# Kernel tuning notes

Hardware: AMD Instinct MI355X
Metric: run time of the kernel (lower is better)

The kernel has to match this reference:

```python
import jax, jax.numpy as jnp
import numpy as np

B, S, D, H, HD = 4096, 50, 32, 4, 8
SCALE = 1.0 / (8 ** 0.5)


def setup_inputs() -> dict:
    key = jax.random.key(0)
    ks = jax.random.split(key, 12)
    inp = {
        'Q': jax.random.normal(ks[0], (B, S, D), dtype=jnp.float32),
        'K': jax.random.normal(ks[1], (B, S, D), dtype=jnp.float32),
        'V': jax.random.normal(ks[2], (B, S, D), dtype=jnp.float32),
        'mask': jax.random.randint(ks[3], (B, 1, S, S), 0, 2).astype(jnp.bool_),
        # Linear weights (stored as [in, out]; equivalent math to torch's x @ W.T + b)
        'WQ': jax.random.normal(ks[4], (D, D), dtype=jnp.float32) * 0.1,
        'bQ': jnp.zeros((D,), dtype=jnp.float32),
        'WK': jax.random.normal(ks[5], (D, D), dtype=jnp.float32) * 0.1,
        'bK': jnp.zeros((D,), dtype=jnp.float32),
        'WV': jax.random.normal(ks[6], (D, D), dtype=jnp.float32) * 0.1,
        'bV': jnp.zeros((D,), dtype=jnp.float32),
        'WO': jax.random.normal(ks[7], (D, D), dtype=jnp.float32) * 0.1,
        'bO': jnp.zeros((D,), dtype=jnp.float32),
    }
    return inp


def reference(Q, K, V, mask, WQ, bQ, WK, bK, WV, bV, WO, bO):
    qSrc = Q
    # fcQ/fcK/fcV are (faithfully) applied twice, as in the original forward
    q = (Q @ WQ + bQ) @ WQ + bQ
    k = (K @ WK + bK) @ WK + bK
    v = (V @ WV + bV) @ WV + bV
    # split heads: [B, S, D] -> [B, H, S, HD]
    q = q.reshape(B, S, H, HD).transpose(0, 2, 1, 3)
    k = k.reshape(B, S, H, HD).transpose(0, 2, 1, 3)
    v = v.reshape(B, S, H, HD).transpose(0, 2, 1, 3)
    score = jnp.einsum('bhqd,bhkd->bhqk', q, k) * SCALE
    score = jnp.where(mask, -jnp.inf, score)
    attn = jax.nn.softmax(score, axis=-1)
    ctx = jnp.einsum('bhqk,bhkd->bhqd', attn, v)
    ctx = ctx.transpose(0, 2, 1, 3).reshape(B, S, D)
    out = ctx @ WO + bO  # dropout is identity in eval mode
    return qSrc + out
```

## Files before the change

### kernel.cpp

```cpp
#include <hip/hip_runtime.h>

#define NB 4096
constexpr float kQscale = 0.35355339059327378f * 1.4426950408889634f;

constexpr int ST = 40;
constexpr int SP = 72;
constexpr int SV = 72;
constexpr int OFF_W  = 0;
constexpr int OFF_V2 = 0;
constexpr int OFF_A  = 5120;
constexpr int OFF_C  = 7680;
constexpr int OFF_B  = 10240;
constexpr int SH_LEN = 12800;

typedef __attribute__((ext_vector_type(8))) short bf16x8;
typedef __attribute__((ext_vector_type(4))) float f32x4;

__device__ __forceinline__ unsigned cvt2(float lo, float hi) {
  unsigned u;
  asm("v_cvt_pk_bf16_f32 %0, %1, %2" : "=v"(u) : "v"(lo), "v"(hi));
  return u;
}
__device__ __forceinline__ float fexp2(float x) {
  float r;
  asm("v_exp_f32 %0, %1" : "=v"(r) : "v"(x));
  return r;
}

__global__ __launch_bounds__(256) void mha(
    const float* __restrict__ Qg, const float* __restrict__ Kg,
    const float* __restrict__ Vg, const void* __restrict__ maskg,
    const float* __restrict__ WQg, const float* __restrict__ bQg,
    const float* __restrict__ WKg, const float* __restrict__ bKg,
    const float* __restrict__ WVg, const float* __restrict__ bVg,
    const float* __restrict__ WOg, const float* __restrict__ bOg,
    float* __restrict__ outg)
{
  __shared__ __align__(16) short SH[SH_LEN];
  __shared__ __align__(16) float sBias[128];
  __shared__ unsigned sRaw[80];
  __shared__ unsigned sMask[128];

  const int t = threadIdx.x;
  const int b = blockIdx.x;
  const int lane = t & 63;
  const int wv = t >> 6;
  const int c = lane & 15, g = lane >> 4;
  const int myrow = wv*16 + c;

  auto stage_tile = [&](const float* __restrict__ src, int dstOff) {
    #pragma unroll
    for (int it = 0; it < 2; ++it) {
      const int idx = t + it*256;
      if (idx < 400) {
        const float4 x = ((const float4*)src)[idx];
        const int s = idx >> 3, qd = idx & 7;
        *(uint2*)&SH[dstOff + s*ST + qd*4] = make_uint2(cvt2(x.x, x.y), cvt2(x.z, x.w));
      }
    }
  };

  auto projStep = [&](bf16x8 xb, int wm, int biasOff, int yOff, float scale) {
    #pragma unroll
    for (int Ni = 0; Ni < 2; ++Ni) {
      const bf16x8 wa = *(const bf16x8*)&SH[OFF_W + wm*1280 + (Ni*16 + c)*ST + g*8];
      const float4 bv = *(const float4*)&sBias[biasOff + Ni*16 + g*4];
      f32x4 acc = {bv.x, bv.y, bv.z, bv.w};
      acc = __builtin_amdgcn_mfma_f32_16x16x32_bf16(wa, xb, acc, 0, 0, 0);
      *(uint2*)&SH[yOff + myrow*ST + Ni*16 + g*4] =
          make_uint2(cvt2(acc[0]*scale, acc[1]*scale), cvt2(acc[2]*scale, acc[3]*scale));
    }
  };

  const unsigned w64det = ((const unsigned*)maskg)[lane];
  unsigned valB[10];
  #pragma unroll
  for (int cc = 0; cc < 10; ++cc) {
    const int idx = (wv*10 + cc)*64 + lane;
    valB[cc] = (idx < 2500) ? (unsigned)((const unsigned char*)maskg)[b*2500 + idx] : 0u;
  }
  stage_tile(Kg + b*1600, OFF_A);
  stage_tile(Qg + b*1600, OFF_C);
  stage_tile(Vg + b*1600, OFF_B);
  #pragma unroll
  for (int m = 0; m < 4; ++m) {
    const float* Wp = (m == 0) ? WQg : (m == 1) ? WKg : (m == 2) ? WVg : WOg;
    const float4 x = ((const float4*)Wp)[t];
    const int k = t >> 3, d0 = (t & 7)*4;
    const unsigned u0 = cvt2(x.x, x.y), u1 = cvt2(x.z, x.w);
    SH[OFF_W + m*1280 + (d0+0)*ST + k] = (short)(u0 & 0xFFFF);
    SH[OFF_W + m*1280 + (d0+1)*ST + k] = (short)(u0 >> 16);
    SH[OFF_W + m*1280 + (d0+2)*ST + k] = (short)(u1 & 0xFFFF);
    SH[OFF_W + m*1280 + (d0+3)*ST + k] = (short)(u1 >> 16);
  }
  if      (t < 32)  sBias[t] = bQg[t];
  else if (t < 64)  sBias[t] = bKg[t-32];
  else if (t < 96)  sBias[t] = bVg[t-64];
  else if (t < 128) sBias[t] = bOg[t-96];
  {
    const bool byteMask = (__ballot(w64det > 1u) != 0ull);
    #pragma unroll
    for (int cc = 0; cc < 10; ++cc) {
      const int ch = wv*10 + cc;
      const int idx = ch*64 + lane;
      unsigned val;
      if (byteMask) val = valB[cc];
      else          val = (idx < 2500) ? ((const unsigned*)maskg)[b*2500 + idx] : 0u;
      const unsigned long long m = __ballot(val != 0u);
      if (lane == 0) {
        sRaw[ch*2]     = (unsigned)m;
        sRaw[ch*2 + 1] = (unsigned)(m >> 32);
      }
    }
  }
  __syncthreads();

  if (t < 100) {
    const int i = t >> 1, half = t & 1;
    const int bitpos = 50*i + half*32;
    const int a = bitpos >> 5, sh = bitpos & 31;
    unsigned w = sRaw[a] >> sh;
    if (sh) w |= sRaw[a+1] << (32 - sh);
    sMask[t] = w;
  }
  {
    const bf16x8 aK = *(const bf16x8*)&SH[OFF_A + myrow*ST + g*8];
    const bf16x8 aV = *(const bf16x8*)&SH[OFF_B + myrow*ST + g*8];
    const bf16x8 aQ = *(const bf16x8*)&SH[OFF_C + myrow*ST + g*8];
    projStep(aK, 1, 32, OFF_A, 1.f);
    projStep(aV, 2, 64, OFF_B, 1.f);
    projStep(aQ, 0, 0,  OFF_C, 1.f);
  }
  f32x4 vacc0, vacc1;
  {
    const bf16x8 aK = *(const bf16x8*)&SH[OFF_A + myrow*ST + g*8];
    const bf16x8 aV = *(const bf16x8*)&SH[OFF_B + myrow*ST + g*8];
    const bf16x8 aQ = *(const bf16x8*)&SH[OFF_C + myrow*ST + g*8];
    projStep(aK, 1, 32, OFF_A, 1.f);
    projStep(aQ, 0, 0, OFF_C, kQscale);
    {
      const bf16x8 b0 = *(const bf16x8*)&SH[OFF_W + 2*1280 + c*ST + g*8];
      const bf16x8 b1 = *(const bf16x8*)&SH[OFF_W + 2*1280 + (16 + c)*ST + g*8];
      const float bv0 = sBias[64 + c], bv1 = sBias[64 + 16 + c];
      f32x4 z0 = {bv0, bv0, bv0, bv0}, z1 = {bv1, bv1, bv1, bv1};
      vacc0 = __builtin_amdgcn_mfma_f32_16x16x32_bf16(aV, b0, z0, 0, 0, 0);
      vacc1 = __builtin_amdgcn_mfma_f32_16x16x32_bf16(aV, b1, z1, 0, 0, 0);
    }
  }
  __syncthreads();

  {
    const int j0 = wv*16 + g*4;
    const float v0 = (j0+0 < 50) ? vacc0[0] : 0.f;
    const float v1 = (j0+1 < 50) ? vacc0[1] : 0.f;
    const float v2 = (j0+2 < 50) ? vacc0[2] : 0.f;
    const float v3 = (j0+3 < 50) ? vacc0[3] : 0.f;
    *(uint2*)&SH[OFF_V2 + c*SV + j0] = make_uint2(cvt2(v0,v1), cvt2(v2,v3));
    const float u0 = (j0+0 < 50) ? vacc1[0] : 0.f;
    const float u1 = (j0+1 < 50) ? vacc1[1] : 0.f;
    const float u2 = (j0+2 < 50) ? vacc1[2] : 0.f;
    const float u3 = (j0+3 < 50) ? vacc1[3] : 0.f;
    *(uint2*)&SH[OFF_V2 + (16 + c)*SV + j0] = make_uint2(cvt2(u0,u1), cvt2(u2,u3));
  }
  const bf16x8 qb = *(const bf16x8*)&SH[OFF_C + myrow*ST + g*8];
  bf16x8 kf[4];
  #pragma unroll
  for (int Ni = 0; Ni < 4; ++Ni)
    kf[Ni] = *(const bf16x8*)&SH[OFF_A + (Ni*16 + c)*ST + g*8];
  const unsigned m0 = (myrow < 50) ? sMask[myrow*2]     : 0xFFFFFFFFu;
  const unsigned m1 = (myrow < 50) ? sMask[myrow*2 + 1] : 0xFFFFFFFFu;
  const bf16x8 zf = {0,0,0,0,0,0,0,0};

  auto qkt_exp = [&](int h, unsigned pk[8], float& ri) {
    const bf16x8 qh = (g == h) ? qb : zf;
    float rs = 0.f;
    #pragma unroll
    for (int Ni = 0; Ni < 4; ++Ni) {
      f32x4 z = {0.f, 0.f, 0.f, 0.f};
      const f32x4 s = __builtin_amdgcn_mfma_f32_16x16x32_bf16(kf[Ni], qh, z, 0, 0, 0);
      const unsigned w = (Ni < 2) ? m0 : m1;
      float p[4];
      #pragma unroll
      for (int r = 0; r < 4; ++r) {
        const int key = Ni*16 + g*4 + r;
        const bool keep = (key < 50) && (((w >> (key & 31)) & 1u) == 0u);
        p[r] = keep ? fexp2(s[r]) : 0.f;
        rs += p[r];
      }
      pk[Ni*2]   = cvt2(p[0], p[1]);
      pk[Ni*2+1] = cvt2(p[2], p[3]);
    }
    rs += __shfl_xor(rs, 16);
    rs += __shfl_xor(rs, 32);
    ri = __builtin_amdgcn_rcpf(rs);
  };

  unsigned pkA[8]; float riA;
  qkt_exp(0, pkA, riA);
  __syncthreads();

  short* SPp = &SH[OFF_A];
  #pragma unroll
  for (int h = 0; h < 4; ++h) {
    #pragma unroll
    for (int Ni = 0; Ni < 4; ++Ni)
      *(uint2*)&SPp[myrow*SP + Ni*16 + g*4] = make_uint2(pkA[Ni*2], pkA[Ni*2+1]);
    const bf16x8 vf0 = *(const bf16x8*)&SH[OFF_V2 + (h*8 + (c & 7))*SV + g*8];
    const bf16x8 vf1 = *(const bf16x8*)&SH[OFF_V2 + (h*8 + (c & 7))*SV + 32 + g*8];
    unsigned pkN[8] = {0,0,0,0,0,0,0,0}; float riN = 0.f;
    if (h < 3) qkt_exp(h+1, pkN, riN);
    const bf16x8 pf0 = *(const bf16x8*)&SPp[myrow*SP + g*8];
    const bf16x8 pf1 = *(const bf16x8*)&SPp[myrow*SP + 32 + g*8];
    f32x4 cac = {0.f, 0.f, 0.f, 0.f};
    cac = __builtin_amdgcn_mfma_f32_16x16x32_bf16(vf0, pf0, cac, 0, 0, 0);
    cac = __builtin_amdgcn_mfma_f32_16x16x32_bf16(vf1, pf1, cac, 0, 0, 0);
    if (g < 2)
      *(uint2*)&SH[OFF_B + myrow*ST + h*8 + g*4] =
          make_uint2(cvt2(cac[0]*riA, cac[1]*riA), cvt2(cac[2]*riA, cac[3]*riA));
    #pragma unroll
    for (int e = 0; e < 8; ++e) pkA[e] = pkN[e];
    riA = riN;
  }

  {
    float res[2][4];
    #pragma unroll
    for (int Nj = 0; Nj < 2; ++Nj)
      #pragma unroll
      for (int r = 0; r < 4; ++r) {
        const int row = wv*16 + g*4 + r;
        res[Nj][r] = (row < 50) ? Qg[b*1600 + row*32 + Nj*16 + c] : 0.f;
      }
    const bf16x8 af = *(const bf16x8*)&SH[OFF_B + myrow*ST + g*8];
    #pragma unroll
    for (int Nj = 0; Nj < 2; ++Nj) {
      const bf16x8 bbf = *(const bf16x8*)&SH[OFF_W + 3*1280 + (Nj*16 + c)*ST + g*8];
      const float bv = sBias[96 + Nj*16 + c];
      f32x4 o = {bv, bv, bv, bv};
      o = __builtin_amdgcn_mfma_f32_16x16x32_bf16(af, bbf, o, 0, 0, 0);
      #pragma unroll
      for (int r = 0; r < 4; ++r) {
        const int row = wv*16 + g*4 + r;
        if (row < 50)
          outg[b*1600 + row*32 + Nj*16 + c] = o[r] + res[Nj][r];
      }
    }
  }
}

extern "C" void kernel_launch(void* const* d_in, const int* in_sizes, int n_in,
                              void* d_out, int out_size, void* d_ws, size_t ws_size,
                              hipStream_t stream) {
  const float* Q  = (const float*)d_in[0];
  const float* K  = (const float*)d_in[1];
  const float* V  = (const float*)d_in[2];
  const void*  M  = d_in[3];
  const float* WQ = (const float*)d_in[4];
  const float* bQ = (const float*)d_in[5];
  const float* WK = (const float*)d_in[6];
  const float* bK = (const float*)d_in[7];
  const float* WV = (const float*)d_in[8];
  const float* bV = (const float*)d_in[9];
  const float* WO = (const float*)d_in[10];
  const float* bO = (const float*)d_in[11];
  float* out = (float*)d_out;
  (void)d_ws; (void)ws_size; (void)in_sizes; (void)n_in; (void)out_size;

  hipLaunchKernelGGL(mha, dim3(NB), dim3(256), 0, stream,
                     Q, K, V, M, WQ, bQ, WK, bK, WV, bV, WO, bO, out);
}
```

Measured before the change: 57.74 us.

## Transpose P and context in registers via permlane swaps instead of LDS

Replaces the shared-memory round trip for the softmax probability matrix and the per-head context output with in-register cross-lane exchanges using v_permlane32/16_swap. The bit mask for each row is now extracted per thread straight from the raw ballot words, which removes the separate sMask staging pass, and weight staging uses coalesced column reads with packed 8-byte LDS stores. This cuts LDS traffic, bank conflicts and one pipelined prefetch structure, but drops the software pipelining of QK^T with PV and relies on the permlane lane mapping being correct.

```diff
diff --git a/kernel.cpp b/kernel.cpp
--- a/kernel.cpp
+++ b/kernel.cpp
@@ -4,7 +4,6 @@
 constexpr float kQscale = 0.35355339059327378f * 1.4426950408889634f;
 
 constexpr int ST = 40;
-constexpr int SP = 72;
 constexpr int SV = 72;
 constexpr int OFF_W  = 0;
 constexpr int OFF_V2 = 0;
@@ -15,6 +14,7 @@
 
 typedef __attribute__((ext_vector_type(8))) short bf16x8;
 typedef __attribute__((ext_vector_type(4))) float f32x4;
+typedef __attribute__((ext_vector_type(4))) unsigned u32x4;
 
 __device__ __forceinline__ unsigned cvt2(float lo, float hi) {
   unsigned u;
@@ -25,6 +25,10 @@
   float r;
   asm("v_exp_f32 %0, %1" : "=v"(r) : "v"(x));
   return r;
+}
+__device__ __forceinline__ void xchF(unsigned& a, unsigned& b) {
+  asm volatile("v_permlane32_swap_b32 %0, %1" : "+v"(a), "+v"(b));
+  asm volatile("v_permlane16_swap_b32 %0, %1" : "+v"(a), "+v"(b));
 }
 
 __global__ __launch_bounds__(256) void mha(
@@ -39,7 +43,6 @@
   __shared__ __align__(16) short SH[SH_LEN];
   __shared__ __align__(16) float sBias[128];
   __shared__ unsigned sRaw[80];
-  __shared__ unsigned sMask[128];
 
   const int t = threadIdx.x;
   const int b = blockIdx.x;
@@ -82,16 +85,17 @@
   stage_tile(Kg + b*1600, OFF_A);
   stage_tile(Qg + b*1600, OFF_C);
   stage_tile(Vg + b*1600, OFF_B);
-  #pragma unroll
-  for (int m = 0; m < 4; ++m) {
-    const float* Wp = (m == 0) ? WQg : (m == 1) ? WKg : (m == 2) ? WVg : WOg;
-    const float4 x = ((const float4*)Wp)[t];
-    const int k = t >> 3, d0 = (t & 7)*4;
-    const unsigned u0 = cvt2(x.x, x.y), u1 = cvt2(x.z, x.w);
-    SH[OFF_W + m*1280 + (d0+0)*ST + k] = (short)(u0 & 0xFFFF);
-    SH[OFF_W + m*1280 + (d0+1)*ST + k] = (short)(u0 >> 16);
-    SH[OFF_W + m*1280 + (d0+2)*ST + k] = (short)(u1 & 0xFFFF);
-    SH[OFF_W + m*1280 + (d0+3)*ST + k] = (short)(u1 >> 16);
+  {
+    const int wd = t & 31, wk0 = (t >> 5) * 4;
+    #pragma unroll
+    for (int m = 0; m < 4; ++m) {
+      const float* Wp = (m == 0) ? WQg : (m == 1) ? WKg : (m == 2) ? WVg : WOg;
+      const float w0 = Wp[(wk0+0)*32 + wd];
+      const float w1 = Wp[(wk0+1)*32 + wd];
+      const float w2 = Wp[(wk0+2)*32 + wd];
+      const float w3 = Wp[(wk0+3)*32 + wd];
+      *(uint2*)&SH[OFF_W + m*1280 + wd*ST + wk0] = make_uint2(cvt2(w0,w1), cvt2(w2,w3));
+    }
   }
   if      (t < 32)  sBias[t] = bQg[t];
   else if (t < 64)  sBias[t] = bKg[t-32];
@@ -115,14 +119,6 @@
   }
   __syncthreads();
 
-  if (t < 100) {
-    const int i = t >> 1, half = t & 1;
-    const int bitpos = 50*i + half*32;
-    const int a = bitpos >> 5, sh = bitpos & 31;
-    unsigned w = sRaw[a] >> sh;
-    if (sh) w |= sRaw[a+1] << (32 - sh);
-    sMask[t] = w;
-  }
   {
     const bf16x8 aK = *(const bf16x8*)&SH[OFF_A + myrow*ST + g*8];
     const bf16x8 aV = *(const bf16x8*)&SH[OFF_B + myrow*ST + g*8];
@@ -138,14 +134,12 @@
     const bf16x8 aQ = *(const bf16x8*)&SH[OFF_C + myrow*ST + g*8];
     projStep(aK, 1, 32, OFF_A, 1.f);
     projStep(aQ, 0, 0, OFF_C, kQscale);
-    {
-      const bf16x8 b0 = *(const bf16x8*)&SH[OFF_W + 2*1280 + c*ST + g*8];
-      const bf16x8 b1 = *(const bf16x8*)&SH[OFF_W + 2*1280 + (16 + c)*ST + g*8];
-      const float bv0 = sBias[64 + c], bv1 = sBias[64 + 16 + c];
-      f32x4 z0 = {bv0, bv0, bv0, bv0}, z1 = {bv1, bv1, bv1, bv1};
-      vacc0 = __builtin_amdgcn_mfma_f32_16x16x32_bf16(aV, b0, z0, 0, 0, 0);
-      vacc1 = __builtin_amdgcn_mfma_f32_16x16x32_bf16(aV, b1, z1, 0, 0, 0);
-    }
+    const bf16x8 b0 = *(const bf16x8*)&SH[OFF_W + 2*1280 + c*ST + g*8];
+    const bf16x8 b1 = *(const bf16x8*)&SH[OFF_W + 2*1280 + (16 + c)*ST + g*8];
+    const float bv0 = sBias[64 + c], bv1 = sBias[64 + 16 + c];
+    f32x4 z0 = {bv0, bv0, bv0, bv0}, z1 = {bv1, bv1, bv1, bv1};
+    vacc0 = __builtin_amdgcn_mfma_f32_16x16x32_bf16(aV, b0, z0, 0, 0, 0);
+    vacc1 = __builtin_amdgcn_mfma_f32_16x16x32_bf16(aV, b1, z1, 0, 0, 0);
   }
   __syncthreads();
 
@@ -162,23 +156,38 @@
     const float u3 = (j0+3 < 50) ? vacc1[3] : 0.f;
     *(uint2*)&SH[OFF_V2 + (16 + c)*SV + j0] = make_uint2(cvt2(u0,u1), cvt2(u2,u3));
   }
+  unsigned mm0, mm1;
+  {
+    const int bp = (myrow < 50) ? 50*myrow : 0;
+    const unsigned ra = sRaw[(bp >> 5) + 0];
+    const unsigned rb = sRaw[(bp >> 5) + 1];
+    const unsigned rc = sRaw[(bp >> 5) + 2];
+    const unsigned sh = bp & 31;
+    mm0 = (unsigned)((((unsigned long long)rb << 32) | ra) >> sh);
+    mm1 = (unsigned)((((unsigned long long)rc << 32) | rb) >> sh);
+    if (myrow >= 50) { mm0 = ~0u; mm1 = ~0u; }
+  }
   const bf16x8 qb = *(const bf16x8*)&SH[OFF_C + myrow*ST + g*8];
   bf16x8 kf[4];
   #pragma unroll
   for (int Ni = 0; Ni < 4; ++Ni)
     kf[Ni] = *(const bf16x8*)&SH[OFF_A + (Ni*16 + c)*ST + g*8];
-  const unsigned m0 = (myrow < 50) ? sMask[myrow*2]     : 0xFFFFFFFFu;
-  const unsigned m1 = (myrow < 50) ? sMask[myrow*2 + 1] : 0xFFFFFFFFu;
+  __syncthreads();
+
   const bf16x8 zf = {0,0,0,0,0,0,0,0};
-
-  auto qkt_exp = [&](int h, unsigned pk[8], float& ri) {
+  unsigned ox0[4], ox1[4];
+  #pragma unroll
+  for (int h = 0; h < 4; ++h) {
+    const bf16x8 vf0 = *(const bf16x8*)&SH[OFF_V2 + (h*8 + (c & 7))*SV + g*8];
+    const bf16x8 vf1 = *(const bf16x8*)&SH[OFF_V2 + (h*8 + (c & 7))*SV + 32 + g*8];
     const bf16x8 qh = (g == h) ? qb : zf;
+    unsigned pk[8];
     float rs = 0.f;
     #pragma unroll
     for (int Ni = 0; Ni < 4; ++Ni) {
       f32x4 z = {0.f, 0.f, 0.f, 0.f};
       const f32x4 s = __builtin_amdgcn_mfma_f32_16x16x32_bf16(kf[Ni], qh, z, 0, 0, 0);
-      const unsigned w = (Ni < 2) ? m0 : m1;
+      const unsigned w = (Ni < 2) ? mm0 : mm1;
       float p[4];
       #pragma unroll
       for (int r = 0; r < 4; ++r) {
@@ -192,34 +201,20 @@
     }
     rs += __shfl_xor(rs, 16);
     rs += __shfl_xor(rs, 32);
-    ri = __builtin_amdgcn_rcpf(rs);
-  };
-
-  unsigned pkA[8]; float riA;
-  qkt_exp(0, pkA, riA);
-  __syncthreads();
-
-  short* SPp = &SH[OFF_A];
-  #pragma unroll
-  for (int h = 0; h < 4; ++h) {
-    #pragma unroll
-    for (int Ni = 0; Ni < 4; ++Ni)
-      *(uint2*)&SPp[myrow*SP + Ni*16 + g*4] = make_uint2(pkA[Ni*2], pkA[Ni*2+1]);
-    const bf16x8 vf0 = *(const bf16x8*)&SH[OFF_V2 + (h*8 + (c & 7))*SV + g*8];
-    const bf16x8 vf1 = *(const bf16x8*)&SH[OFF_V2 + (h*8 + (c & 7))*SV + 32 + g*8];
-    unsigned pkN[8] = {0,0,0,0,0,0,0,0}; float riN = 0.f;
-    if (h < 3) qkt_exp(h+1, pkN, riN);
-    const bf16x8 pf0 = *(const bf16x8*)&SPp[myrow*SP + g*8];
-    const bf16x8 pf1 = *(const bf16x8*)&SPp[myrow*SP + 32 + g*8];
+    const float ri = __builtin_amdgcn_rcpf(rs);
+    unsigned w0 = pk[0], w2 = pk[2];  xchF(w0, w2);
+    unsigned w1 = pk[1], w3 = pk[3];  xchF(w1, w3);
+    unsigned x0 = pk[4], x2 = pk[6];  xchF(x0, x2);
+    unsigned x1 = pk[5], x3 = pk[7];  xchF(x1, x3);
+    const u32x4 w0v = {w0, w1, w2, w3};
+    const u32x4 w1v = {x0, x1, x2, x3};
+    const bf16x8 pf0 = __builtin_bit_cast(bf16x8, w0v);
+    const bf16x8 pf1 = __builtin_bit_cast(bf16x8, w1v);
     f32x4 cac = {0.f, 0.f, 0.f, 0.f};
     cac = __builtin_amdgcn_mfma_f32_16x16x32_bf16(vf0, pf0, cac, 0, 0, 0);
     cac = __builtin_amdgcn_mfma_f32_16x16x32_bf16(vf1, pf1, cac, 0, 0, 0);
-    if (g < 2)
-      *(uint2*)&SH[OFF_B + myrow*ST + h*8 + g*4] =
-          make_uint2(cvt2(cac[0]*riA, cac[1]*riA), cvt2(cac[2]*riA, cac[3]*riA));
-    #pragma unroll
-    for (int e = 0; e < 8; ++e) pkA[e] = pkN[e];
-    riA = riN;
+    ox0[h] = cvt2(cac[0]*ri, cac[1]*ri);
+    ox1[h] = cvt2(cac[2]*ri, cac[3]*ri);
   }
 
   {
@@ -231,7 +226,18 @@
         const int row = wv*16 + g*4 + r;
         res[Nj][r] = (row < 50) ? Qg[b*1600 + row*32 + Nj*16 + c] : 0.f;
       }
-    const bf16x8 af = *(const bf16x8*)&SH[OFF_B + myrow*ST + g*8];
+    unsigned a0 = ox0[0], a1 = ox0[1], a2 = ox0[2], a3 = ox0[3];
+    xchF(a0, a1);
+    xchF(a2, a3);
+    xchF(a0, a2);
+    xchF(a1, a3);
+    unsigned c0 = ox1[0], c1 = ox1[1], c2 = ox1[2], c3 = ox1[3];
+    xchF(c0, c1);
+    xchF(c2, c3);
+    xchF(c0, c2);
+    xchF(c1, c3);
+    const u32x4 afv = {a0, c0, a1, c1};
+    const bf16x8 af = __builtin_bit_cast(bf16x8, afv);
     #pragma unroll
     for (int Nj = 0; Nj < 2; ++Nj) {
       const bf16x8 bbf = *(const bf16x8*)&SH[OFF_W + 3*1280 + (Nj*16 + c)*ST + g*8];
```

After: 56.46 us. 2.2% less time.
